# Performance work log

Measured on AMD Instinct MI355X. Metric: run time of the kernel, lower is better.

Reference implementation:

```python
import jax, jax.numpy as jnp
import numpy as np

NUM_HEADS = 16
HEAD_DIM = 64
HIDDEN = NUM_HEADS * HEAD_DIM  # 1024
Q_DIM = 512
KV_DIM = 256


def setup_inputs() -> dict:
    key = jax.random.key(0)
    k1, k2, k3, k4, k5, k6 = jax.random.split(key, 6)
    B, I, J = 64, 128, 512  # num_assets, num_latents, window_size
    q = jax.random.normal(k1, (B, I, Q_DIM), dtype=jnp.float32)
    kv = jax.random.normal(k2, (B, J, KV_DIM), dtype=jnp.float32)
    # Linear weights stored as (in, out); fan-in scaled init
    Wq = jax.random.normal(k3, (Q_DIM, HIDDEN), dtype=jnp.float32) / np.sqrt(Q_DIM)
    Wkv = jax.random.normal(k4, (KV_DIM, 2 * HIDDEN), dtype=jnp.float32) / np.sqrt(KV_DIM)
    Wo = jax.random.normal(k5, (HIDDEN, Q_DIM), dtype=jnp.float32) / np.sqrt(HIDDEN)
    bo = jax.random.normal(k6, (Q_DIM,), dtype=jnp.float32) * 0.01
    return {"q": q, "kv": kv, "Wq": Wq, "Wkv": Wkv, "Wo": Wo, "bo": bo}


def reference(q, kv, Wq, Wkv, Wo, bo):
    B, I, _ = q.shape
    J = kv.shape[1]
    scale = HEAD_DIM ** -0.5
    query = q @ Wq                              # (B, I, HIDDEN)
    k, v = jnp.split(kv @ Wkv, 2, axis=-1)      # each (B, J, HIDDEN)
    qh = query.reshape(B, I, NUM_HEADS, HEAD_DIM).transpose(0, 2, 1, 3)  # bhid
    kh = k.reshape(B, J, NUM_HEADS, HEAD_DIM).transpose(0, 2, 1, 3)      # bhjd
    vh = v.reshape(B, J, NUM_HEADS, HEAD_DIM).transpose(0, 2, 1, 3)      # bhjd
    scores = jnp.einsum('bhid,bhjd->bhij', qh, kh) * scale
    attn = jax.nn.softmax(scores, axis=-1)
    out = jnp.einsum('bhij,bhjd->bhid', attn, vh)
    out = out.transpose(0, 2, 1, 3).reshape(B, I, HIDDEN)
    return out @ Wo + bo
```

## Files before the change

### kernel.cpp

```cpp
#include <hip/hip_runtime.h>
#include <stdint.h>

typedef unsigned short ushort_t;
typedef __attribute__((ext_vector_type(8))) short short8;
typedef __attribute__((ext_vector_type(4))) float floatx4;
typedef __attribute__((ext_vector_type(4))) float floatv4;
typedef __attribute__((ext_vector_type(4))) unsigned short ushortv4;


__device__ __forceinline__ ushort_t f2bf(float x) {
    union { float f; unsigned u; } v; v.f = x;
    unsigned r = v.u + 0x7fffu + ((v.u >> 16) & 1u);
    return (ushort_t)(r >> 16);
}

__device__ __forceinline__ void gl_lds16(const ushort_t* g, ushort_t* l) {
    __builtin_amdgcn_global_load_lds(
        (const __attribute__((address_space(1))) void*)g,
        (__attribute__((address_space(3))) void*)l, 16, 0, 0);
}

__global__ __launch_bounds__(256) void prep_kernel(
    const float* __restrict__ q, const float* __restrict__ kv,
    const float* __restrict__ Wq, const float* __restrict__ Wkv,
    const float* __restrict__ Wo,
    ushort_t* __restrict__ qA, ushort_t* __restrict__ kvA,
    ushort_t* __restrict__ WqT, ushort_t* __restrict__ WkvT,
    ushort_t* __restrict__ WoT)
{
    const int bid = blockIdx.x;
    const int tid = threadIdx.x;
    if (bid < 4096) {
        int t = bid * 256 + tid;
        floatv4 v = ((const floatv4*)q)[t];
        ushortv4 o;
        o[0] = f2bf(v[0]); o[1] = f2bf(v[1]); o[2] = f2bf(v[2]); o[3] = f2bf(v[3]);
        ((ushortv4*)qA)[t] = o;
    } else if (bid < 12288) {
        int t = (bid - 4096) * 256 + tid;
        floatv4 v = ((const floatv4*)kv)[t];
        ushortv4 o;
        o[0] = f2bf(v[0]); o[1] = f2bf(v[1]); o[2] = f2bf(v[2]); o[3] = f2bf(v[3]);
        ((ushortv4*)kvA)[t] = o;
    } else if (bid < 14336) {
        int t = (bid - 12288) * 256 + tid;
        int n = t >> 9, k = t & 511;
        WqT[t] = f2bf(Wq[k * 1024 + n] * 0.125f);
    } else if (bid < 16384) {
        int t = (bid - 14336) * 256 + tid;
        int n = t >> 8, k = t & 255;
        WkvT[t] = f2bf(Wkv[k * 2048 + n]);
    } else {
        int t = (bid - 16384) * 256 + tid;
        int n = t >> 10, k = t & 1023;
        WoT[t] = f2bf(Wo[k * 512 + n]);
    }
}

__global__ __launch_bounds__(256, 3) void gemm_bt_kernel(
    const ushort_t* __restrict__ A, const ushort_t* __restrict__ Bt,
    int M, int N, int K, int gx, int gy, int emode,
    ushort_t* __restrict__ out_a,
    float* __restrict__ out_f, const float* __restrict__ bias)
{
    __shared__ ushort_t smem[16896];
    ushort_t* sA = smem;
    ushort_t* sB = smem + 8192;
    ushort_t* sT = smem;

    const int bid  = blockIdx.x;
    const int xcd  = bid & 7;
    const int slot = bid >> 3;
    const int band = gy >> 3;
    const int by   = xcd * band + slot % band;
    const int bx   = slot / band;

    const int tid  = threadIdx.x;
    const int lane = tid & 63;
    const int w    = tid >> 6;
    const int quad = lane >> 4;
    const int l15  = lane & 15;
    const int wr   = w >> 1, wc = w & 1;
    const int m0 = by * 128;
    const int n0 = bx * 128;

    const int rsub = lane >> 3;
    const int c8   = lane & 7;
    const int wrow = w * 32;

    floatx4 acc[4][4];
#pragma unroll
    for (int i = 0; i < 4; i++)
#pragma unroll
        for (int j = 0; j < 4; j++) acc[i][j] = (floatx4){0.f, 0.f, 0.f, 0.f};

    for (int k0 = 0; k0 < K; k0 += 64) {
        __syncthreads();
#pragma unroll
        for (int t = 0; t < 4; t++) {
            int rg = wrow + t * 8;
            gl_lds16(&A[(size_t)(m0 + rg + rsub) * K + k0 + c8 * 8], &sA[rg * 64]);
            gl_lds16(&Bt[(size_t)(n0 + rg + rsub) * K + k0 + c8 * 8], &sB[rg * 64]);
        }
        __syncthreads();
#pragma unroll
        for (int ks = 0; ks < 64; ks += 32) {
            short8 af[4], bf[4];
#pragma unroll
            for (int i = 0; i < 4; i++)
                af[i] = *(const short8*)&sA[(wr * 64 + i * 16 + l15) * 64 + ks + quad * 8];
#pragma unroll
            for (int j = 0; j < 4; j++)
                bf[j] = *(const short8*)&sB[(wc * 64 + j * 16 + l15) * 64 + ks + quad * 8];
#pragma unroll
            for (int i = 0; i < 4; i++)
#pragma unroll
                for (int j = 0; j < 4; j++)
                    acc[i][j] = __builtin_amdgcn_mfma_f32_16x16x32_bf16(
                        af[i], bf[j], acc[i][j], 0, 0, 0);
        }
    }

    if (emode == 2) {
#pragma unroll
        for (int i = 0; i < 4; i++)
#pragma unroll
            for (int j = 0; j < 4; j++)
#pragma unroll
                for (int r = 0; r < 4; r++) {
                    int grow = m0 + wr * 64 + i * 16 + quad * 4 + r;
                    int gcol = n0 + wc * 64 + j * 16 + l15;
                    out_f[(size_t)grow * N + gcol] = acc[i][j][r] + bias[gcol];
                }
        return;
    }

    __syncthreads();
#pragma unroll
    for (int i = 0; i < 4; i++)
#pragma unroll
        for (int j = 0; j < 4; j++)
#pragma unroll
            for (int r = 0; r < 4; r++) {
                int row = wr * 64 + i * 16 + quad * 4 + r;
                int col = wc * 64 + j * 16 + l15;
                sT[row * 132 + col] = f2bf(acc[i][j][r]);
            }
    __syncthreads();
#pragma unroll
    for (int it = 0; it < 8; it++) {
        int idx = it * 256 + tid;
        int row = idx >> 4, chunk = idx & 15;
        short8 v = *(const short8*)&sT[row * 132 + chunk * 8];
        *(short8*)&out_a[(size_t)(m0 + row) * 1024 + n0 + chunk * 8] = v;
    }
}

__global__ __launch_bounds__(512, 4) void fattn_kernel(
    const ushort_t* __restrict__ Q,
    const ushort_t* __restrict__ KV,
    const ushort_t* __restrict__ W,
    ushort_t* __restrict__ O)
{
    __shared__ ushort_t sKV[64 * 264];
    __shared__ ushort_t sKc[64 * 72];
    __shared__ ushort_t sVt[64 * 72];
    __shared__ ushort_t sP[8 * 16 * 72];

    const int bid  = blockIdx.x;
    const int xcd  = bid & 7;
    const int slot = bid >> 3;
    const int b = xcd * 8 + (slot & 7);
    const int h = slot >> 3;

    const int tid  = threadIdx.x;
    const int lane = tid & 63, w = tid >> 6;
    const int quad = lane >> 4, l15 = lane & 15;

    short8 wf[8];
    {
        int n = w * 16 + l15;
        int grow = (n < 64) ? (h * 64 + n) : (1024 + h * 64 + (n - 64));
        const ushort_t* wp = &W[(size_t)grow * 256 + quad * 8];
#pragma unroll
        for (int ks = 0; ks < 8; ks++)
            wf[ks] = *(const short8*)(wp + ks * 32);
    }

    const ushort_t* qrow = &Q[(size_t)(b * 128 + w * 16 + l15) * 1024 + h * 64 + quad * 8];
    short8 aq0 = *(const short8*)qrow;
    short8 aq1 = *(const short8*)(qrow + 32);

    float lsum[4];
    floatx4 acc_o[4];
#pragma unroll
    for (int r = 0; r < 4; r++) lsum[r] = 0.f;
#pragma unroll
    for (int dt = 0; dt < 4; dt++) acc_o[dt] = (floatx4){0.f, 0.f, 0.f, 0.f};

    ushort_t* sp = &sP[w * 1152];

    for (int ch = 0; ch < 8; ch++) {
        const int j0 = ch * 64;
#pragma unroll
        for (int t = 0; t < 4; t++) {
            int c = tid + t * 512;
            int row = c >> 5, cc = c & 31;
            *(short8*)&sKV[row * 264 + cc * 8] =
                *(const short8*)&KV[(size_t)(b * 512 + j0 + row) * 256 + cc * 8];
        }
        __syncthreads();

        floatx4 pacc[4];
#pragma unroll
        for (int jt = 0; jt < 4; jt++) pacc[jt] = (floatx4){0.f, 0.f, 0.f, 0.f};
#pragma unroll
        for (int ks = 0; ks < 8; ks++) {
            short8 af[4];
#pragma unroll
            for (int jt = 0; jt < 4; jt++)
                af[jt] = *(const short8*)&sKV[(jt * 16 + l15) * 264 + ks * 32 + quad * 8];
#pragma unroll
            for (int jt = 0; jt < 4; jt++)
                pacc[jt] = __builtin_amdgcn_mfma_f32_16x16x32_bf16(
                    af[jt], wf[ks], pacc[jt], 0, 0, 0);
        }

        if (w < 4) {
            int d = w * 16 + l15;
#pragma unroll
            for (int jt = 0; jt < 4; jt++)
#pragma unroll
                for (int r = 0; r < 4; r++)
                    sKc[(jt * 16 + quad * 4 + r) * 72 + d] = f2bf(pacc[jt][r]);
        } else {
            int d = (w - 4) * 16 + l15;
#pragma unroll
            for (int jt = 0; jt < 4; jt++) {
                ushortv4 p;
#pragma unroll
                for (int r = 0; r < 4; r++) p[r] = f2bf(pacc[jt][r]);
                *(ushortv4*)&sVt[d * 72 + jt * 16 + quad * 4] = p;
            }
        }
        __syncthreads();

#pragma unroll
        for (int jt = 0; jt < 4; jt++) {
            const ushort_t* kp = &sKc[(jt * 16 + l15) * 72 + quad * 8];
            short8 bk0 = *(const short8*)kp;
            short8 bk1 = *(const short8*)(kp + 32);
            floatx4 a = (floatx4){0.f, 0.f, 0.f, 0.f};
            a = __builtin_amdgcn_mfma_f32_16x16x32_bf16(aq0, bk0, a, 0, 0, 0);
            a = __builtin_amdgcn_mfma_f32_16x16x32_bf16(aq1, bk1, a, 0, 0, 0);
            ushortv4 pk;
#pragma unroll
            for (int r = 0; r < 4; r++) {
                float p = __expf(a[r]);
                lsum[r] += p;
                pk[r] = f2bf(p);
            }
#pragma unroll
            for (int r = 0; r < 4; r++)
                sp[(quad * 4 + r) * 72 + jt * 16 + l15] = pk[r];
        }

#pragma unroll
        for (int kk = 0; kk < 2; kk++) {
            short8 ap = *(const short8*)&sp[l15 * 72 + kk * 32 + quad * 8];
#pragma unroll
            for (int dt = 0; dt < 4; dt++) {
                short8 bv = *(const short8*)&sVt[(dt * 16 + l15) * 72 + kk * 32 + quad * 8];
                acc_o[dt] = __builtin_amdgcn_mfma_f32_16x16x32_bf16(ap, bv, acc_o[dt], 0, 0, 0);
            }
        }
    }

#pragma unroll
    for (int r = 0; r < 4; r++) {
        float s = lsum[r];
#pragma unroll
        for (int off = 1; off < 16; off <<= 1) s += __shfl_xor(s, off);
        float inv = 1.0f / s;
        size_t rowo = (size_t)(b * 128 + w * 16 + quad * 4 + r) * 1024 + h * 64;
#pragma unroll
        for (int dt = 0; dt < 4; dt++)
            O[rowo + dt * 16 + l15] = f2bf(acc_o[dt][r] * inv);
    }
}

extern "C" void kernel_launch(void* const* d_in, const int* in_sizes, int n_in,
                              void* d_out, int out_size, void* d_ws, size_t ws_size,
                              hipStream_t stream) {
    const float* q   = (const float*)d_in[0];
    const float* kv  = (const float*)d_in[1];
    const float* Wq  = (const float*)d_in[2];
    const float* Wkv = (const float*)d_in[3];
    const float* Wo  = (const float*)d_in[4];
    const float* bo  = (const float*)d_in[5];
    float* out = (float*)d_out;

    char* ws = (char*)d_ws;
    ushort_t* qA    = (ushort_t*)(ws + 0);
    ushort_t* kvA   = (ushort_t*)(ws + 8388608);
    ushort_t* WqT   = (ushort_t*)(ws + 25165824);
    ushort_t* WkvT  = (ushort_t*)(ws + 26214400);
    ushort_t* WoT   = (ushort_t*)(ws + 27262976);
    ushort_t* qraw  = (ushort_t*)(ws + 28311552);
    ushort_t* attnO = (ushort_t*)(ws + 45088768);

    hipLaunchKernelGGL(prep_kernel, dim3(18432), dim3(256), 0, stream,
                       q, kv, Wq, Wkv, Wo, qA, kvA, WqT, WkvT, WoT);

    hipLaunchKernelGGL(gemm_bt_kernel, dim3(512), dim3(256), 0, stream,
                       qA, WqT, 8192, 1024, 512, 8, 64, 0, qraw,
                       (float*)nullptr, (const float*)nullptr);
    hipLaunchKernelGGL(fattn_kernel, dim3(1024), dim3(512), 0, stream,
                       qraw, kvA, WkvT, attnO);
    hipLaunchKernelGGL(gemm_bt_kernel, dim3(256), dim3(256), 0, stream,
                       attnO, WoT, 8192, 512, 1024, 4, 64, 2, (ushort_t*)nullptr,
                       out, bo);
}
```

Measured before the change: 219.9 us.

## Fuse Q projection into attention kernel and tile weight transposes via LDS

Removes the separate Q-projection GEMM launch. The attention kernel now computes each (batch, head) query tile directly from bf16 q and the transposed Wq slice using MFMA, staging both through shared memory, so the qraw round-trip through global memory goes away. The weight transpose in the prep kernel now uses 64x64 LDS tiles with vectorized coalesced reads and writes instead of strided scalar reads, which cuts its block count. The cost is that Q is recomputed per head block and the attention kernel's prologue and shared-memory footprint grow.

```diff
diff --git a/kernel.cpp b/kernel.cpp
--- a/kernel.cpp
+++ b/kernel.cpp
@@ -28,6 +28,7 @@
     ushort_t* __restrict__ WqT, ushort_t* __restrict__ WkvT,
     ushort_t* __restrict__ WoT)
 {
+    __shared__ ushort_t tileS[64 * 68];
     const int bid = blockIdx.x;
     const int tid = threadIdx.x;
     if (bid < 4096) {
@@ -36,24 +37,39 @@
         ushortv4 o;
         o[0] = f2bf(v[0]); o[1] = f2bf(v[1]); o[2] = f2bf(v[2]); o[3] = f2bf(v[3]);
         ((ushortv4*)qA)[t] = o;
-    } else if (bid < 12288) {
+        return;
+    }
+    if (bid < 12288) {
         int t = (bid - 4096) * 256 + tid;
         floatv4 v = ((const floatv4*)kv)[t];
         ushortv4 o;
         o[0] = f2bf(v[0]); o[1] = f2bf(v[1]); o[2] = f2bf(v[2]); o[3] = f2bf(v[3]);
         ((ushortv4*)kvA)[t] = o;
-    } else if (bid < 14336) {
-        int t = (bid - 12288) * 256 + tid;
-        int n = t >> 9, k = t & 511;
-        WqT[t] = f2bf(Wq[k * 1024 + n] * 0.125f);
-    } else if (bid < 16384) {
-        int t = (bid - 14336) * 256 + tid;
-        int n = t >> 8, k = t & 255;
-        WkvT[t] = f2bf(Wkv[k * 2048 + n]);
-    } else {
-        int t = (bid - 16384) * 256 + tid;
-        int n = t >> 10, k = t & 1023;
-        WoT[t] = f2bf(Wo[k * 512 + n]);
+        return;
+    }
+    const float* src; ushort_t* dst; int K, N, kt, nt; float scale = 1.0f;
+    if (bid < 12416)      { int tl = bid - 12288; src = Wq;  dst = WqT;  K = 512;  N = 1024; kt = tl >> 4; nt = tl & 15; scale = 0.125f; }
+    else if (bid < 12544) { int tl = bid - 12416; src = Wkv; dst = WkvT; K = 256;  N = 2048; kt = tl >> 5; nt = tl & 31; }
+    else                  { int tl = bid - 12544; src = Wo;  dst = WoT;  K = 1024; N = 512;  kt = tl >> 3; nt = tl & 7;  }
+#pragma unroll
+    for (int t = 0; t < 4; t++) {
+        int e = t * 256 + tid;
+        int row = e >> 4, c4 = e & 15;
+        floatv4 v = *(const floatv4*)&src[(size_t)(kt * 64 + row) * N + nt * 64 + c4 * 4];
+        ushortv4 o;
+        o[0] = f2bf(v[0] * scale); o[1] = f2bf(v[1] * scale);
+        o[2] = f2bf(v[2] * scale); o[3] = f2bf(v[3] * scale);
+        *(ushortv4*)&tileS[row * 68 + c4 * 4] = o;
+    }
+    __syncthreads();
+#pragma unroll
+    for (int t = 0; t < 4; t++) {
+        int e = t * 256 + tid;
+        int orow = e >> 4, c4 = e & 15;
+        ushortv4 o;
+#pragma unroll
+        for (int e2 = 0; e2 < 4; e2++) o[e2] = tileS[(c4 * 4 + e2) * 68 + orow];
+        *(ushortv4*)&dst[(size_t)(nt * 64 + orow) * K + kt * 64 + c4 * 4] = o;
     }
 }
 
@@ -157,15 +173,19 @@
 }
 
 __global__ __launch_bounds__(512, 4) void fattn_kernel(
-    const ushort_t* __restrict__ Q,
+    const ushort_t* __restrict__ QA,
+    const ushort_t* __restrict__ WQ,
     const ushort_t* __restrict__ KV,
     const ushort_t* __restrict__ W,
     ushort_t* __restrict__ O)
 {
-    __shared__ ushort_t sKV[64 * 264];
-    __shared__ ushort_t sKc[64 * 72];
-    __shared__ ushort_t sVt[64 * 72];
-    __shared__ ushort_t sP[8 * 16 * 72];
+    __shared__ ushort_t smem[35328];
+    ushort_t* sKV = smem;
+    ushort_t* sKc = smem + 16896;
+    ushort_t* sVt = smem + 21504;
+    ushort_t* sP  = smem + 26112;
+    ushort_t* sQ  = smem;
+    ushort_t* sW  = smem + 17408;
 
     const int bid  = blockIdx.x;
     const int xcd  = bid & 7;
@@ -177,6 +197,51 @@
     const int lane = tid & 63, w = tid >> 6;
     const int quad = lane >> 4, l15 = lane & 15;
 
+    ushort_t* sp = &sP[w * 1152];
+
+    const ushort_t* qb = &QA[(size_t)b * 128 * 512];
+    const ushort_t* wq = &WQ[(size_t)h * 64 * 512];
+    floatx4 qacc[4];
+#pragma unroll
+    for (int nt = 0; nt < 4; nt++) qacc[nt] = (floatx4){0.f, 0.f, 0.f, 0.f};
+
+    for (int kc = 0; kc < 4; kc++) {
+        if (kc) __syncthreads();
+#pragma unroll
+        for (int t = 0; t < 4; t++) {
+            int c = tid + t * 512;
+            int row = c >> 4, cc = c & 15;
+            *(short8*)&sQ[row * 136 + cc * 8] =
+                *(const short8*)&qb[(size_t)row * 512 + kc * 128 + cc * 8];
+        }
+#pragma unroll
+        for (int t = 0; t < 2; t++) {
+            int c = tid + t * 512;
+            int row = c >> 4, cc = c & 15;
+            *(short8*)&sW[row * 136 + cc * 8] =
+                *(const short8*)&wq[(size_t)row * 512 + kc * 128 + cc * 8];
+        }
+        __syncthreads();
+#pragma unroll
+        for (int ks = 0; ks < 4; ks++) {
+            short8 af = *(const short8*)&sQ[(w * 16 + l15) * 136 + ks * 32 + quad * 8];
+#pragma unroll
+            for (int nt = 0; nt < 4; nt++) {
+                short8 bfr = *(const short8*)&sW[(nt * 16 + l15) * 136 + ks * 32 + quad * 8];
+                qacc[nt] = __builtin_amdgcn_mfma_f32_16x16x32_bf16(af, bfr, qacc[nt], 0, 0, 0);
+            }
+        }
+    }
+    __syncthreads();
+
+#pragma unroll
+    for (int nt = 0; nt < 4; nt++)
+#pragma unroll
+        for (int r = 0; r < 4; r++)
+            sp[(quad * 4 + r) * 72 + nt * 16 + l15] = f2bf(qacc[nt][r]);
+    short8 aq0 = *(const short8*)&sp[l15 * 72 + quad * 8];
+    short8 aq1 = *(const short8*)&sp[l15 * 72 + 32 + quad * 8];
+
     short8 wf[8];
     {
         int n = w * 16 + l15;
@@ -187,18 +252,12 @@
             wf[ks] = *(const short8*)(wp + ks * 32);
     }
 
-    const ushort_t* qrow = &Q[(size_t)(b * 128 + w * 16 + l15) * 1024 + h * 64 + quad * 8];
-    short8 aq0 = *(const short8*)qrow;
-    short8 aq1 = *(const short8*)(qrow + 32);
-
     float lsum[4];
     floatx4 acc_o[4];
 #pragma unroll
     for (int r = 0; r < 4; r++) lsum[r] = 0.f;
 #pragma unroll
     for (int dt = 0; dt < 4; dt++) acc_o[dt] = (floatx4){0.f, 0.f, 0.f, 0.f};
-
-    ushort_t* sp = &sP[w * 1152];
 
     for (int ch = 0; ch < 8; ch++) {
         const int j0 = ch * 64;
@@ -306,17 +365,14 @@
     ushort_t* WqT   = (ushort_t*)(ws + 25165824);
     ushort_t* WkvT  = (ushort_t*)(ws + 26214400);
     ushort_t* WoT   = (ushort_t*)(ws + 27262976);
-    ushort_t* qraw  = (ushort_t*)(ws + 28311552);
     ushort_t* attnO = (ushort_t*)(ws + 45088768);
 
-    hipLaunchKernelGGL(prep_kernel, dim3(18432), dim3(256), 0, stream,
+    hipLaunchKernelGGL(prep_kernel, dim3(12672), dim3(256), 0, stream,
                        q, kv, Wq, Wkv, Wo, qA, kvA, WqT, WkvT, WoT);
 
-    hipLaunchKernelGGL(gemm_bt_kernel, dim3(512), dim3(256), 0, stream,
-                       qA, WqT, 8192, 1024, 512, 8, 64, 0, qraw,
-                       (float*)nullptr, (const float*)nullptr);
     hipLaunchKernelGGL(fattn_kernel, dim3(1024), dim3(512), 0, stream,
-                       qraw, kvA, WkvT, attnO);
+                       qA, WqT, kvA, WkvT, attnO);
+
     hipLaunchKernelGGL(gemm_bt_kernel, dim3(256), dim3(256), 0, stream,
                        attnO, WoT, 8192, 512, 1024, 4, 64, 2, (ushort_t*)nullptr,
                        out, bo);
```

After: 213.4 us. 1.03x faster.
